# Performance work log

Measured on AMD Instinct MI355X. Metric: run time of the kernel, lower is better.

## Reference

```python
import jax, jax.numpy as jnp
import numpy as np
import math

LOG2PI = math.log(2.0 * math.pi)

def _silu(x):
    return x * jax.nn.sigmoid(x)

def _gru(x, W_ih, W_hh, b_ih, b_hh):
    # x: [B,T,X]; torch nn.GRU single layer, batch_first
    B = x.shape[0]
    H = W_hh.shape[1]
    gi_all = jnp.einsum('btx,gx->btg', x, W_ih) + b_ih  # [B,T,3H] input gates precomputed
    def step(h, gi):
        gh = h @ W_hh.T + b_hh
        i_r, i_z, i_n = jnp.split(gi, 3, axis=-1)
        h_r, h_z, h_n = jnp.split(gh, 3, axis=-1)
        r = jax.nn.sigmoid(i_r + h_r)
        z = jax.nn.sigmoid(i_z + h_z)
        n = jnp.tanh(i_n + r * h_n)
        h_new = (1.0 - z) * n + z * h
        return h_new, h_new
    h0 = jnp.zeros((B, H), x.dtype)
    h_last, h_seq = jax.lax.scan(step, h0, jnp.swapaxes(gi_all, 0, 1))
    return jnp.swapaxes(h_seq, 0, 1), h_last  # [B,T,H], [B,H]

def _A_Q(kappa, sigma, dt):
    A = jnp.exp(-kappa * dt)
    two_k_dt = 2.0 * kappa * dt
    small = (two_k_dt < 1e-6).astype(dt.dtype)
    Q_exact = sigma ** 2 * (1.0 - jnp.exp(-two_k_dt)) / jnp.maximum(2.0 * kappa, 1e-12)
    Q_taylor = sigma ** 2 * dt * (1.0 - kappa * dt + two_k_dt ** 2 / 6.0)
    Q = small * Q_taylor + (1.0 - small) * Q_exact
    return A, Q

def _ou_posterior(m0, s0, mu_k, A_k, Q_k, eps0, eps):
    B, Tm1, C = mu_k.shape
    c0 = m0 + s0 * eps0  # [B,C]
    s0c = jnp.maximum(s0, 1e-12)
    log_q0 = -0.5 * (((c0 - m0) / s0c) ** 2 + 2.0 * jnp.log(s0c) + LOG2PI).sum(-1)
    noise = eps * jnp.sqrt(jnp.maximum(Q_k, 1e-12))
    b = (1.0 - A_k) * mu_k + noise
    Phi_prefix = jnp.cumprod(A_k, axis=1)  # [B,T-1,C]
    Phi_full = jnp.concatenate([jnp.ones((B, 1, C), mu_k.dtype), Phi_prefix], axis=1)
    denom = jnp.maximum(Phi_full[:, 1:, :], 1e-20)
    s = b / denom
    S_full = jnp.concatenate([jnp.zeros((B, 1, C), mu_k.dtype), jnp.cumsum(s, axis=1)], axis=1)
    c = Phi_full * (c0[:, None, :] + S_full)  # [B,T,C]
    mean_trans = mu_k + A_k * (c[:, :-1, :] - mu_k)
    var_trans = jnp.maximum(Q_k, 1e-12)
    log_q_trans = -0.5 * ((c[:, 1:, :] - mean_trans) ** 2 / var_trans + jnp.log(var_trans) + LOG2PI)
    log_q = log_q0 + log_q_trans.sum(-1).sum(-1)
    return c, log_q

def reference(x, t, eps0, eps, W_ih, W_hh, b_ih, b_hh, Wi1, bi1, Wi2, bi2, Ws1, bs1, Ws2, bs2, Ws3, bs3):
    B, T, _ = x.shape
    h_seq, h_global = _gru(x, W_ih, W_hh, b_ih, b_hh)
    # soft time attention, temperature = 1.0
    delta = t[:, :, None, 0] - t[:, None, :, 0]  # [B,T,T]
    logits = -(T * delta) ** 2  # / tau^2 with tau=1
    w = jax.nn.softmax(logits, axis=-1)
    attn = jnp.einsum('bkj,bjh->bkh', w, h_seq)
    # init head
    h0_ctx = h_global + attn[:, 0, :]
    hi = _silu(h0_ctx @ Wi1.T + bi1)
    m0, logs0 = jnp.split(hi @ Wi2.T + bi2, 2, axis=-1)
    s0 = jax.nn.softplus(logs0) + 1e-6
    # step head on ctx[:, :-1]
    ctx = jnp.concatenate([h_global[:, None, :] + attn, t], axis=-1)[:, :-1, :]
    hs = _silu(ctx @ Ws1.T + bs1)
    hs = _silu(hs @ Ws2.T + bs2)
    params = hs @ Ws3.T + bs3
    mu_k, logk_k, logs_k = jnp.split(params, 3, axis=-1)
    kappa_k = jax.nn.softplus(logk_k) + 1e-6
    sigma_k = jax.nn.softplus(logs_k) + 1e-6
    dt = jnp.maximum(t[:, 1:, :] - t[:, :-1, :], 1e-6)
    A_k, Q_k = _A_Q(kappa_k, sigma_k, dt)
    c, log_q = _ou_posterior(m0, s0, mu_k, A_k, Q_k, eps0, eps)
    return c, log_q

def setup_inputs() -> dict:
    B, T, X, H, C = 8, 2048, 64, 256, 32
    key = jax.random.key(0)
    ks = jax.random.split(key, 16)
    def w(k, shape, scale=0.02):
        return (scale * jax.random.normal(k, shape)).astype(jnp.float32)
    x = jax.random.normal(ks[0], (B, T, X), dtype=jnp.float32)
    t = jnp.sort(jax.random.uniform(ks[1], (B, T, 1), dtype=jnp.float32), axis=1)
    eps0 = jax.random.normal(ks[2], (B, C), dtype=jnp.float32)
    eps = jax.random.normal(ks[3], (B, T - 1, C), dtype=jnp.float32)
    return {
        'x': x, 't': t, 'eps0': eps0, 'eps': eps,
        'W_ih': w(ks[4], (3 * H, X)), 'W_hh': w(ks[5], (3 * H, H)),
        'b_ih': jnp.zeros((3 * H,), jnp.float32), 'b_hh': jnp.zeros((3 * H,), jnp.float32),
        'Wi1': w(ks[6], (H, H)), 'bi1': jnp.zeros((H,), jnp.float32),
        'Wi2': w(ks[7], (2 * C, H)), 'bi2': jnp.zeros((2 * C,), jnp.float32),
        'Ws1': w(ks[8], (H, H + 1)), 'bs1': jnp.zeros((H,), jnp.float32),
        'Ws2': w(ks[9], (H, H)), 'bs2': jnp.zeros((H,), jnp.float32),
        'Ws3': w(ks[10], (3 * C, H)), 'bs3': jnp.zeros((3 * C,), jnp.float32),
    }
```

## Files before the change

kernel.cpp:

```cpp
#include <hip/hip_runtime.h>
#include <hip/hip_fp16.h>

#define LOG2PI_F 1.8378770664093453f

typedef _Float16 hf2_t __attribute__((ext_vector_type(2)));

#if defined(__has_builtin)
#  if __has_builtin(__builtin_amdgcn_fdot2)
#    define USE_FDOT2 1
#  endif
#endif
#ifndef USE_FDOT2
#  define USE_FDOT2 0
#endif

__device__ __forceinline__ float fdot2(unsigned int a, unsigned int b, float c) {
#if USE_FDOT2
  return __builtin_amdgcn_fdot2(__builtin_bit_cast(hf2_t, a),
                                __builtin_bit_cast(hf2_t, b), c, false);
#else
  __half2 ha = __builtin_bit_cast(__half2, a);
  __half2 hb = __builtin_bit_cast(__half2, b);
  float2 fa = __half22float2(ha);
  float2 fb = __half22float2(hb);
  return c + fa.x * fb.x + fa.y * fb.y;
#endif
}

__device__ __forceinline__ unsigned int packh2(float lo, float hi) {
  unsigned int l = (unsigned int)__half_as_ushort(__float2half(lo));
  unsigned int h = (unsigned int)__half_as_ushort(__float2half(hi));
  return (h << 16) | l;
}

__device__ __forceinline__ float sigmoid_f(float x) { return 1.f / (1.f + __expf(-x)); }
__device__ __forceinline__ float silu_f(float x) { return x * sigmoid_f(x); }
__device__ __forceinline__ float softplus_f(float x) {
  return fmaxf(x, 0.f) + log1pf(__expf(-fabsf(x)));
}
__device__ __forceinline__ float tanh_f(float x) {
  float ax = fabsf(x);
  float e = __expf(2.f * ax);
  return copysignf(1.f - 2.f / (e + 1.f), x);
}

__global__ void transpose_k(const float* __restrict__ in, float* __restrict__ out,
                            int R, int C) {
  int i = blockIdx.x * 256 + threadIdx.x;
  if (i < R * C) {
    int r = i / C, c = i % C;
    out[c * R + r] = in[i];
  }
}

__global__ void whh_pack(const float* __restrict__ W, unsigned int* __restrict__ WpkT) {
  int i = blockIdx.x * 256 + threadIdx.x;
  if (i < 98304) {
    int d = i / 768, g = i % 768;
    float lo = W[g * 256 + 2 * d];
    float hi = W[g * 256 + 2 * d + 1];
    WpkT[i] = packh2(lo, hi);
  }
}

__global__ void gi_gemm(const float* __restrict__ x, const float* __restrict__ WT,
                        const float* __restrict__ bih, float* __restrict__ gi) {
  int m0 = blockIdx.x * 8;
  int g = threadIdx.x;
  __shared__ float xs[8][64];
  for (int i = g; i < 512; i += 256) xs[i >> 6][i & 63] = x[m0 * 64 + i];
  __syncthreads();
  float b0 = bih[g], b1 = bih[g + 256], b2 = bih[g + 512];
  float a0[8], a1[8], a2[8];
#pragma unroll
  for (int r = 0; r < 8; r++) { a0[r] = b0; a1[r] = b1; a2[r] = b2; }
  for (int k = 0; k < 64; k++) {
    const float* w = WT + k * 768;
    float w0 = w[g], w1 = w[g + 256], w2 = w[g + 512];
#pragma unroll
    for (int r = 0; r < 8; r++) {
      float xv = xs[r][k];
      a0[r] = fmaf(w0, xv, a0[r]);
      a1[r] = fmaf(w1, xv, a1[r]);
      a2[r] = fmaf(w2, xv, a2[r]);
    }
  }
#pragma unroll
  for (int r = 0; r < 8; r++) {
    float* o = gi + (m0 + r) * 768;
    o[g] = a0[r];
    o[g + 256] = a1[r];
    o[g + 512] = a2[r];
  }
}

__global__ __launch_bounds__(768, 3) void gru_kernel(
    const unsigned int* __restrict__ WpkT,
    const float* __restrict__ gi,
    const float* __restrict__ bhh,
    float* __restrict__ h_seq)
{
  const int b = blockIdx.x;
  const int g = threadIdx.x;

  uint4 w[32];
#pragma unroll
  for (int i = 0; i < 32; i++) {
    int d = 4 * i;
    w[i] = make_uint4(WpkT[(d + 0) * 768 + g], WpkT[(d + 1) * 768 + g],
                      WpkT[(d + 2) * 768 + g], WpkT[(d + 3) * 768 + g]);
  }

  __shared__ __align__(16) unsigned int hpk[2][128];
  __shared__ float als[1024];
  if (g < 128) hpk[0][g] = 0u;

  const float bb = bhh[g];
  float h = 0.f;
  const float* gib = gi + b * 2048 * 768;
  float* hsb = h_seq + b * 2048 * 256;
  float gcur = gib[g];
  __syncthreads();

  for (int t = 0; t < 2048; t++) {
    float gnext = gib[min(t + 1, 2047) * 768 + g];

    const uint4* hp = (const uint4*)hpk[t & 1];
    float a = bb;
#pragma unroll
    for (int i = 0; i < 32; i++) {
      uint4 hv = hp[i];
      a = fdot2(w[i].x, hv.x, a);
      a = fdot2(w[i].y, hv.y, a);
      a = fdot2(w[i].z, hv.z, a);
      a = fdot2(w[i].w, hv.w, a);
    }
    if (g < 512) {
      als[g] = a + gcur;
    } else {
      als[g] = a;
      als[g + 256] = gcur;
    }
    __syncthreads();

    if (g < 256) {
      float rv = sigmoid_f(als[g]);
      float zv = sigmoid_f(als[256 + g]);
      float nv = tanh_f(als[768 + g] + rv * als[512 + g]);
      float hn = (1.f - zv) * nv + zv * h;
      h = hn;
      hsb[t * 256 + g] = hn;
      float other = __shfl_xor(hn, 1);
      if ((g & 1) == 0) hpk[(t + 1) & 1][g >> 1] = packh2(hn, other);
    }
    gcur = gnext;
    __syncthreads();
  }
}

#define AW 80
__global__ void attn_kernel(const float* __restrict__ h_seq, const float* __restrict__ t,
                            float* __restrict__ ctx) {
  const int blk = blockIdx.x;
  const int b = blk >> 7;
  const int k0 = (blk & 127) << 4;
  const int tid = threadIdx.x;

  __shared__ __align__(16) float ewT[176][16];
  __shared__ float ts[176];
  __shared__ float tks[16];
  __shared__ float rden[16];

  const float* tb = t + b * 2048;
  if (tid < 176) {
    int j = k0 - AW + tid;
    ts[tid] = tb[min(max(j, 0), 2047)];
  }
  if (tid < 16) tks[tid] = tb[k0 + tid];
  __syncthreads();

  for (int p = tid; p < 176 * 16; p += 256) {
    int kk = p & 15, jr = p >> 4;
    int j = k0 - AW + jr;
    float d = 2048.f * (tks[kk] - ts[jr]);
    float e = (j >= 0 && j < 2048) ? __expf(-d * d) : 0.f;
    ewT[jr][kk] = e;
  }
  __syncthreads();

  if (tid < 16) {
    float s = 0.f;
    for (int jr = 0; jr < 176; jr++) s += ewT[jr][tid];
    rden[tid] = 1.f / s;
  }
  __syncthreads();

  float acc[16];
#pragma unroll
  for (int kk = 0; kk < 16; kk++) acc[kk] = 0.f;

  const float* hb = h_seq + b * 2048 * 256;
  for (int jr = 0; jr < 176; jr++) {
    int j = min(max(k0 - AW + jr, 0), 2047);
    float hv = hb[j * 256 + tid];
    const float4* e4 = (const float4*)ewT[jr];
    float4 e0 = e4[0], e1 = e4[1], e2 = e4[2], e3 = e4[3];
    acc[0] = fmaf(e0.x, hv, acc[0]);   acc[1] = fmaf(e0.y, hv, acc[1]);
    acc[2] = fmaf(e0.z, hv, acc[2]);   acc[3] = fmaf(e0.w, hv, acc[3]);
    acc[4] = fmaf(e1.x, hv, acc[4]);   acc[5] = fmaf(e1.y, hv, acc[5]);
    acc[6] = fmaf(e1.z, hv, acc[6]);   acc[7] = fmaf(e1.w, hv, acc[7]);
    acc[8] = fmaf(e2.x, hv, acc[8]);   acc[9] = fmaf(e2.y, hv, acc[9]);
    acc[10] = fmaf(e2.z, hv, acc[10]); acc[11] = fmaf(e2.w, hv, acc[11]);
    acc[12] = fmaf(e3.x, hv, acc[12]); acc[13] = fmaf(e3.y, hv, acc[13]);
    acc[14] = fmaf(e3.z, hv, acc[14]); acc[15] = fmaf(e3.w, hv, acc[15]);
  }

  float hg = hb[2047 * 256 + tid];
  float* cb = ctx + (b * 2048 + k0) * 256 + tid;
#pragma unroll
  for (int kk = 0; kk < 16; kk++) cb[kk * 256] = hg + acc[kk] * rden[kk];
}

__global__ void init_head(const float* __restrict__ ctx, const float* __restrict__ WT1,
                          const float* __restrict__ bi1, const float* __restrict__ WT2,
                          const float* __restrict__ bi2, const float* __restrict__ eps0,
                          float* __restrict__ m0s0, float* __restrict__ lq0) {
  int b = blockIdx.x;
  int g = threadIdx.x;
  __shared__ float xs[256], his[256], ms[64], red[32];
  xs[g] = ctx[(b * 2048) * 256 + g];
  __syncthreads();
  float acc = bi1[g];
#pragma unroll 8
  for (int k = 0; k < 256; k++) acc = fmaf(WT1[k * 256 + g], xs[k], acc);
  his[g] = silu_f(acc);
  __syncthreads();
  if (g < 64) {
    float a2 = bi2[g];
#pragma unroll 8
    for (int k = 0; k < 256; k++) a2 = fmaf(WT2[k * 64 + g], his[k], a2);
    float v = (g < 32) ? a2 : (softplus_f(a2) + 1e-6f);
    m0s0[b * 64 + g] = v;
    ms[g] = v;
  }
  __syncthreads();
  if (g < 32) {
    float m = ms[g], s = ms[32 + g];
    float c0 = m + s * eps0[b * 32 + g];
    float sc = fmaxf(s, 1e-12f);
    float z = (c0 - m) / sc;
    red[g] = z * z + 2.f * __logf(sc) + LOG2PI_F;
  }
  __syncthreads();
  if (g == 0) {
    float s = 0.f;
    for (int i = 0; i < 32; i++) s += red[i];
    lq0[b] = -0.5f * s;
  }
}

__global__ void head_layer(const float* __restrict__ A, const float* __restrict__ WT,
                           const float* __restrict__ bias, const float* __restrict__ wext,
                           const float* __restrict__ tvec, float* __restrict__ C,
                           int N, int act) {
  int m0 = blockIdx.x * 8;
  int g = threadIdx.x;
  __shared__ __align__(16) float As[8][256];
#pragma unroll
  for (int r = 0; r < 8; r++) As[r][g] = A[(m0 + r) * 256 + g];
  __syncthreads();
  if (g < N) {
    float b0 = bias[g];
    float acc[8] = {b0, b0, b0, b0, b0, b0, b0, b0};
    for (int k4 = 0; k4 < 64; k4++) {
      const float* w = WT + (k4 * 4) * N + g;
      float w0v = w[0], w1v = w[N], w2v = w[2 * N], w3v = w[3 * N];
#pragma unroll
      for (int r = 0; r < 8; r++) {
        float4 xv = *(const float4*)(&As[r][k4 * 4]);
        acc[r] = fmaf(w0v, xv.x, acc[r]);
        acc[r] = fmaf(w1v, xv.y, acc[r]);
        acc[r] = fmaf(w2v, xv.z, acc[r]);
        acc[r] = fmaf(w3v, xv.w, acc[r]);
      }
    }
#pragma unroll
    for (int r = 0; r < 8; r++) {
      float a = acc[r];
      if (wext) a = fmaf(tvec[m0 + r], wext[g], a);
      if (act) a = silu_f(a);
      C[(m0 + r) * N + g] = a;
    }
  }
}

__global__ __launch_bounds__(1024) void ou_kernel(
    const float* __restrict__ params, const float* __restrict__ t,
    const float* __restrict__ eps, const float* __restrict__ eps0,
    const float* __restrict__ m0s0, const float* __restrict__ lq0,
    float* __restrict__ out) {
  const int b = blockIdx.x;
  const int c = threadIdx.x & 31;
  const int s = threadIdx.x >> 5;
  const int k0 = s * 64;
  const int k1 = min(k0 + 64, 2047);
  const float* tb = t + b * 2048;

  __shared__ float Ps[32][33], Ss[32][33], Cs[32][33], lqs[32][33];

  float P = 1.f, S = 0.f, lq = 0.f;
  for (int k = k0; k < k1; k++) {
    const float* pr = params + (b * 2048 + k) * 96;
    float mu = pr[c];
    float kap = softplus_f(pr[32 + c]) + 1e-6f;
    float sg = softplus_f(pr[64 + c]) + 1e-6f;
    float dt = fmaxf(tb[k + 1] - tb[k], 1e-6f);
    float A = __expf(-kap * dt);
    float tkd = 2.f * kap * dt;
    float Qe = sg * sg * (1.f - A * A) / fmaxf(2.f * kap, 1e-12f);
    float kd = kap * dt;
    float Qt = sg * sg * dt * (1.f - kd + tkd * tkd * (1.f / 6.f));
    float var = fmaxf((tkd < 1e-6f) ? Qt : Qe, 1e-12f);
    float e = eps[(b * 2047 + k) * 32 + c];
    float d = mu * (1.f - A) + e * sqrtf(var);
    S = fmaf(A, S, d);
    P *= A;
    lq += e * e + __logf(var) + LOG2PI_F;
  }
  Ps[c][s] = P;
  Ss[c][s] = S;
  lqs[c][s] = lq;
  __syncthreads();

  if (s == 0) {
    float m0v = m0s0[b * 64 + c];
    float s0v = m0s0[b * 64 + 32 + c];
    float cc = fmaf(s0v, eps0[b * 32 + c], m0v);
    out[(b * 2048) * 32 + c] = cc;
    float lqt = 0.f;
    for (int i = 0; i < 32; i++) {
      Cs[c][i] = cc;
      cc = fmaf(Ps[c][i], cc, Ss[c][i]);
      lqt += lqs[c][i];
    }
    for (int off = 16; off >= 1; off >>= 1) lqt += __shfl_down(lqt, off, 32);
    if (c == 0) out[8 * 2048 * 32 + b] = lq0[b] - 0.5f * lqt;
  }
  __syncthreads();

  float cc = Cs[c][s];
  for (int k = k0; k < k1; k++) {
    const float* pr = params + (b * 2048 + k) * 96;
    float mu = pr[c];
    float kap = softplus_f(pr[32 + c]) + 1e-6f;
    float sg = softplus_f(pr[64 + c]) + 1e-6f;
    float dt = fmaxf(tb[k + 1] - tb[k], 1e-6f);
    float A = __expf(-kap * dt);
    float tkd = 2.f * kap * dt;
    float Qe = sg * sg * (1.f - A * A) / fmaxf(2.f * kap, 1e-12f);
    float kd = kap * dt;
    float Qt = sg * sg * dt * (1.f - kd + tkd * tkd * (1.f / 6.f));
    float var = fmaxf((tkd < 1e-6f) ? Qt : Qe, 1e-12f);
    float e = eps[(b * 2047 + k) * 32 + c];
    float d = mu * (1.f - A) + e * sqrtf(var);
    cc = fmaf(A, cc, d);
    out[(b * 2048 + k + 1) * 32 + c] = cc;
  }
}

extern "C" void kernel_launch(void* const* d_in, const int* in_sizes, int n_in,
                              void* d_out, int out_size, void* d_ws, size_t ws_size,
                              hipStream_t stream) {
  (void)in_sizes; (void)n_in; (void)out_size; (void)ws_size;
  const float* x    = (const float*)d_in[0];
  const float* t    = (const float*)d_in[1];
  const float* eps0 = (const float*)d_in[2];
  const float* eps  = (const float*)d_in[3];
  const float* W_ih = (const float*)d_in[4];
  const float* W_hh = (const float*)d_in[5];
  const float* b_ih = (const float*)d_in[6];
  const float* b_hh = (const float*)d_in[7];
  const float* Wi1  = (const float*)d_in[8];
  const float* bi1  = (const float*)d_in[9];
  const float* Wi2  = (const float*)d_in[10];
  const float* bi2  = (const float*)d_in[11];
  const float* Ws1  = (const float*)d_in[12];
  const float* bs1  = (const float*)d_in[13];
  const float* Ws2  = (const float*)d_in[14];
  const float* bs2  = (const float*)d_in[15];
  const float* Ws3  = (const float*)d_in[16];
  const float* bs3  = (const float*)d_in[17];
  float* out = (float*)d_out;
  float* ws = (float*)d_ws;

  float*        WT_ih = ws + 0;
  unsigned int* WpkT  = (unsigned int*)(ws + 49152);
  float*        WT1   = ws + 147456;
  float*        WT2   = ws + 212992;
  float*        WTs1  = ws + 229376;
  float*        WTs2  = ws + 295168;
  float*        WTs3  = ws + 360704;
  float*        m0s0  = ws + 385280;
  float*        lq0   = ws + 385792;
  float*        gi    = ws + 385800;
  float*        h_seq = gi + 12582912;
  float*        ctx   = h_seq + 4194304;
  float*        hs1    = gi;
  float*        hs2    = gi + 4194304;
  float*        params = gi + 8388608;

  transpose_k<<<(768 * 64 + 255) / 256, 256, 0, stream>>>(W_ih, WT_ih, 768, 64);
  transpose_k<<<(256 * 256 + 255) / 256, 256, 0, stream>>>(Wi1, WT1, 256, 256);
  transpose_k<<<(64 * 256 + 255) / 256, 256, 0, stream>>>(Wi2, WT2, 64, 256);
  transpose_k<<<(256 * 257 + 255) / 256, 256, 0, stream>>>(Ws1, WTs1, 256, 257);
  transpose_k<<<(256 * 256 + 255) / 256, 256, 0, stream>>>(Ws2, WTs2, 256, 256);
  transpose_k<<<(96 * 256 + 255) / 256, 256, 0, stream>>>(Ws3, WTs3, 96, 256);
  whh_pack<<<384, 256, 0, stream>>>(W_hh, WpkT);

  gi_gemm<<<2048, 256, 0, stream>>>(x, WT_ih, b_ih, gi);
  gru_kernel<<<8, 768, 0, stream>>>(WpkT, gi, b_hh, h_seq);
  attn_kernel<<<1024, 256, 0, stream>>>(h_seq, t, ctx);
  init_head<<<8, 256, 0, stream>>>(ctx, WT1, bi1, WT2, bi2, eps0, m0s0, lq0);
  head_layer<<<2048, 256, 0, stream>>>(ctx, WTs1, bs1, WTs1 + 256 * 256, t, hs1, 256, 1);
  head_layer<<<2048, 256, 0, stream>>>(hs1, WTs2, bs2, nullptr, nullptr, hs2, 256, 1);
  head_layer<<<2048, 256, 0, stream>>>(hs2, WTs3, bs3, nullptr, nullptr, params, 96, 0);
  ou_kernel<<<8, 1024, 0, stream>>>(params, t, eps, eps0, m0s0, lq0, out);
}
```

Before: 3.156 ms.

## Fuse weight prep and head MLP layers, split GRU hidden n-gate across 512 threads

Merges the seven weight transpose/pack launches into one prep kernel. Fuses the three head MLP layers with the per-step OU coefficient computation, so intermediates stay in shared memory and the OU kernel only reads precomputed A, D and log terms instead of recomputing softplus/exp twice. Reworks the GRU recurrence to use 512 threads per block instead of 768, with each thread computing one full gate row plus half of an n-gate row, and the r gate kept in registers. The GRU change adds register pressure (48 uint4 per thread) and an extra shared-memory sum for the split dot product.

```diff
diff --git a/kernel.cpp b/kernel.cpp
--- a/kernel.cpp
+++ b/kernel.cpp
@@ -44,22 +44,39 @@
   return copysignf(1.f - 2.f / (e + 1.f), x);
 }
 
-__global__ void transpose_k(const float* __restrict__ in, float* __restrict__ out,
-                            int R, int C) {
-  int i = blockIdx.x * 256 + threadIdx.x;
+__device__ __forceinline__ void tr_piece(const float* in, float* out, int R, int C,
+                                         int i) {
   if (i < R * C) {
     int r = i / C, c = i % C;
     out[c * R + r] = in[i];
   }
 }
 
-__global__ void whh_pack(const float* __restrict__ W, unsigned int* __restrict__ WpkT) {
-  int i = blockIdx.x * 256 + threadIdx.x;
-  if (i < 98304) {
-    int d = i / 768, g = i % 768;
-    float lo = W[g * 256 + 2 * d];
-    float hi = W[g * 256 + 2 * d + 1];
-    WpkT[i] = packh2(lo, hi);
+__global__ void prep_kernel(const float* W_ih, const float* Wi1, const float* Wi2,
+                            const float* Ws1, const float* Ws2, const float* Ws3,
+                            const float* W_hh, float* WT_ih, float* WT1, float* WT2,
+                            float* WTs1, float* WTs2, float* WTs3,
+                            unsigned int* WpkT) {
+  int blk = blockIdx.x;
+  int tid = threadIdx.x;
+  if (blk < 192) {
+    tr_piece(W_ih, WT_ih, 768, 64, blk * 256 + tid);
+  } else if (blk < 448) {
+    tr_piece(Wi1, WT1, 256, 256, (blk - 192) * 256 + tid);
+  } else if (blk < 512) {
+    tr_piece(Wi2, WT2, 64, 256, (blk - 448) * 256 + tid);
+  } else if (blk < 769) {
+    tr_piece(Ws1, WTs1, 256, 257, (blk - 512) * 256 + tid);
+  } else if (blk < 1025) {
+    tr_piece(Ws2, WTs2, 256, 256, (blk - 769) * 256 + tid);
+  } else if (blk < 1121) {
+    tr_piece(Ws3, WTs3, 96, 256, (blk - 1025) * 256 + tid);
+  } else {
+    int i = (blk - 1121) * 256 + tid;
+    if (i < 98304) {
+      int d = i / 768, g = i % 768;
+      WpkT[i] = packh2(W_hh[g * 256 + 2 * d], W_hh[g * 256 + 2 * d + 1]);
+    }
   }
 }
 
@@ -94,66 +111,121 @@
   }
 }
 
-__global__ __launch_bounds__(768, 3) void gru_kernel(
+__global__ __launch_bounds__(512, 2) void gru_kernel(
     const unsigned int* __restrict__ WpkT,
     const float* __restrict__ gi,
     const float* __restrict__ bhh,
     float* __restrict__ h_seq)
 {
   const int b = blockIdx.x;
-  const int g = threadIdx.x;
-
-  uint4 w[32];
+  const int tid = threadIdx.x;
+  const int d = tid & 255;
+  const int half = tid >> 8;
+  const int nrow = 512 + d;
+
+  uint4 wf[32], wh[16];
 #pragma unroll
   for (int i = 0; i < 32; i++) {
-    int d = 4 * i;
-    w[i] = make_uint4(WpkT[(d + 0) * 768 + g], WpkT[(d + 1) * 768 + g],
-                      WpkT[(d + 2) * 768 + g], WpkT[(d + 3) * 768 + g]);
+    int dk = 4 * i;
+    wf[i] = make_uint4(WpkT[(dk + 0) * 768 + tid], WpkT[(dk + 1) * 768 + tid],
+                       WpkT[(dk + 2) * 768 + tid], WpkT[(dk + 3) * 768 + tid]);
+  }
+#pragma unroll
+  for (int i = 0; i < 16; i++) {
+    int dk = half * 64 + 4 * i;
+    wh[i] = make_uint4(WpkT[(dk + 0) * 768 + nrow], WpkT[(dk + 1) * 768 + nrow],
+                       WpkT[(dk + 2) * 768 + nrow], WpkT[(dk + 3) * 768 + nrow]);
+  }
+#pragma unroll
+  for (int i = 0; i < 32; i++) {
+    asm volatile("" : "+v"(wf[i].x), "+v"(wf[i].y), "+v"(wf[i].z), "+v"(wf[i].w));
+  }
+#pragma unroll
+  for (int i = 0; i < 16; i++) {
+    asm volatile("" : "+v"(wh[i].x), "+v"(wh[i].y), "+v"(wh[i].z), "+v"(wh[i].w));
   }
 
   __shared__ __align__(16) unsigned int hpk[2][128];
-  __shared__ float als[1024];
-  if (g < 128) hpk[0][g] = 0u;
-
-  const float bb = bhh[g];
+  __shared__ float als[768];
+  if (tid < 128) hpk[0][tid] = 0u;
+
+  const float bf = bhh[tid];
+  const float bh = (half == 0) ? bhh[nrow] : 0.f;
   float h = 0.f;
   const float* gib = gi + b * 2048 * 768;
   float* hsb = h_seq + b * 2048 * 256;
-  float gcur = gib[g];
+  float gcur = gib[tid];
+  float gncur = (tid < 256) ? gib[512 + tid] : 0.f;
   __syncthreads();
 
   for (int t = 0; t < 2048; t++) {
-    float gnext = gib[min(t + 1, 2047) * 768 + g];
+    int tn = min(t + 1, 2047);
+    float gnext = gib[tn * 768 + tid];
+    float gnnext = (tid < 256) ? gib[tn * 768 + 512 + tid] : 0.f;
 
     const uint4* hp = (const uint4*)hpk[t & 1];
-    float a = bb;
-#pragma unroll
-    for (int i = 0; i < 32; i++) {
-      uint4 hv = hp[i];
-      a = fdot2(w[i].x, hv.x, a);
-      a = fdot2(w[i].y, hv.y, a);
-      a = fdot2(w[i].z, hv.z, a);
-      a = fdot2(w[i].w, hv.w, a);
-    }
-    if (g < 512) {
-      als[g] = a + gcur;
+    float af = bf, ah = bh;
+    if (half == 0) {
+#pragma unroll
+      for (int i = 0; i < 16; i++) {
+        uint4 hv = hp[i];
+        af = fdot2(wf[i].x, hv.x, af);
+        af = fdot2(wf[i].y, hv.y, af);
+        af = fdot2(wf[i].z, hv.z, af);
+        af = fdot2(wf[i].w, hv.w, af);
+        ah = fdot2(wh[i].x, hv.x, ah);
+        ah = fdot2(wh[i].y, hv.y, ah);
+        ah = fdot2(wh[i].z, hv.z, ah);
+        ah = fdot2(wh[i].w, hv.w, ah);
+      }
+#pragma unroll
+      for (int i = 16; i < 32; i++) {
+        uint4 hv = hp[i];
+        af = fdot2(wf[i].x, hv.x, af);
+        af = fdot2(wf[i].y, hv.y, af);
+        af = fdot2(wf[i].z, hv.z, af);
+        af = fdot2(wf[i].w, hv.w, af);
+      }
     } else {
-      als[g] = a;
-      als[g + 256] = gcur;
-    }
+#pragma unroll
+      for (int i = 0; i < 16; i++) {
+        uint4 hv = hp[i];
+        af = fdot2(wf[i].x, hv.x, af);
+        af = fdot2(wf[i].y, hv.y, af);
+        af = fdot2(wf[i].z, hv.z, af);
+        af = fdot2(wf[i].w, hv.w, af);
+      }
+#pragma unroll
+      for (int i = 16; i < 32; i++) {
+        uint4 hv = hp[i];
+        af = fdot2(wf[i].x, hv.x, af);
+        af = fdot2(wf[i].y, hv.y, af);
+        af = fdot2(wf[i].z, hv.z, af);
+        af = fdot2(wf[i].w, hv.w, af);
+        ah = fdot2(wh[i - 16].x, hv.x, ah);
+        ah = fdot2(wh[i - 16].y, hv.y, ah);
+        ah = fdot2(wh[i - 16].z, hv.z, ah);
+        ah = fdot2(wh[i - 16].w, hv.w, ah);
+      }
+    }
+
+    if (tid >= 256) als[tid - 256] = af + gcur;
+    als[256 + tid] = ah;
     __syncthreads();
 
-    if (g < 256) {
-      float rv = sigmoid_f(als[g]);
-      float zv = sigmoid_f(als[256 + g]);
-      float nv = tanh_f(als[768 + g] + rv * als[512 + g]);
+    if (tid < 256) {
+      float rv = sigmoid_f(af + gcur);
+      float zv = sigmoid_f(als[d]);
+      float npart = als[256 + d] + als[512 + d];
+      float nv = tanh_f(gncur + rv * npart);
       float hn = (1.f - zv) * nv + zv * h;
       h = hn;
-      hsb[t * 256 + g] = hn;
+      hsb[t * 256 + d] = hn;
       float other = __shfl_xor(hn, 1);
-      if ((g & 1) == 0) hpk[(t + 1) & 1][g >> 1] = packh2(hn, other);
+      if ((d & 1) == 0) hpk[(t + 1) & 1][d >> 1] = packh2(hn, other);
     }
     gcur = gnext;
+    gncur = gnnext;
     __syncthreads();
   }
 }
@@ -259,22 +331,31 @@
   }
 }
 
-__global__ void head_layer(const float* __restrict__ A, const float* __restrict__ WT,
-                           const float* __restrict__ bias, const float* __restrict__ wext,
-                           const float* __restrict__ tvec, float* __restrict__ C,
-                           int N, int act) {
+__global__ __launch_bounds__(256) void head_fused(
+    const float* __restrict__ ctx, const float* __restrict__ WTs1,
+    const float* __restrict__ bs1, const float* __restrict__ WTs2,
+    const float* __restrict__ bs2, const float* __restrict__ WTs3,
+    const float* __restrict__ bs3, const float* __restrict__ t,
+    const float* __restrict__ eps, float* __restrict__ Aarr,
+    float* __restrict__ Darr, float* __restrict__ Larr) {
   int m0 = blockIdx.x * 8;
   int g = threadIdx.x;
   __shared__ __align__(16) float As[8][256];
-#pragma unroll
-  for (int r = 0; r < 8; r++) As[r][g] = A[(m0 + r) * 256 + g];
-  __syncthreads();
-  if (g < N) {
-    float b0 = bias[g];
+  __shared__ __align__(16) float Bs[8][256];
+  __shared__ float Ps[8][96];
+  __shared__ float trow[8];
+
+#pragma unroll
+  for (int r = 0; r < 8; r++) As[r][g] = ctx[(m0 + r) * 256 + g];
+  if (g < 8) trow[g] = t[m0 + g];
+  __syncthreads();
+
+  {
+    float b0 = bs1[g];
     float acc[8] = {b0, b0, b0, b0, b0, b0, b0, b0};
     for (int k4 = 0; k4 < 64; k4++) {
-      const float* w = WT + (k4 * 4) * N + g;
-      float w0v = w[0], w1v = w[N], w2v = w[2 * N], w3v = w[3 * N];
+      const float* w = WTs1 + (k4 * 4) * 256 + g;
+      float w0v = w[0], w1v = w[256], w2v = w[512], w3v = w[768];
 #pragma unroll
       for (int r = 0; r < 8; r++) {
         float4 xv = *(const float4*)(&As[r][k4 * 4]);
@@ -284,19 +365,79 @@
         acc[r] = fmaf(w3v, xv.w, acc[r]);
       }
     }
-#pragma unroll
-    for (int r = 0; r < 8; r++) {
-      float a = acc[r];
-      if (wext) a = fmaf(tvec[m0 + r], wext[g], a);
-      if (act) a = silu_f(a);
-      C[(m0 + r) * N + g] = a;
+    float we = WTs1[256 * 256 + g];
+#pragma unroll
+    for (int r = 0; r < 8; r++) Bs[r][g] = silu_f(fmaf(trow[r], we, acc[r]));
+  }
+  __syncthreads();
+
+  {
+    float b0 = bs2[g];
+    float acc[8] = {b0, b0, b0, b0, b0, b0, b0, b0};
+    for (int k4 = 0; k4 < 64; k4++) {
+      const float* w = WTs2 + (k4 * 4) * 256 + g;
+      float w0v = w[0], w1v = w[256], w2v = w[512], w3v = w[768];
+#pragma unroll
+      for (int r = 0; r < 8; r++) {
+        float4 xv = *(const float4*)(&Bs[r][k4 * 4]);
+        acc[r] = fmaf(w0v, xv.x, acc[r]);
+        acc[r] = fmaf(w1v, xv.y, acc[r]);
+        acc[r] = fmaf(w2v, xv.z, acc[r]);
+        acc[r] = fmaf(w3v, xv.w, acc[r]);
+      }
+    }
+#pragma unroll
+    for (int r = 0; r < 8; r++) As[r][g] = silu_f(acc[r]);
+  }
+  __syncthreads();
+
+  if (g < 96) {
+    float b0 = bs3[g];
+    float acc[8] = {b0, b0, b0, b0, b0, b0, b0, b0};
+    for (int k4 = 0; k4 < 64; k4++) {
+      const float* w = WTs3 + (k4 * 4) * 96 + g;
+      float w0v = w[0], w1v = w[96], w2v = w[192], w3v = w[288];
+#pragma unroll
+      for (int r = 0; r < 8; r++) {
+        float4 xv = *(const float4*)(&As[r][k4 * 4]);
+        acc[r] = fmaf(w0v, xv.x, acc[r]);
+        acc[r] = fmaf(w1v, xv.y, acc[r]);
+        acc[r] = fmaf(w2v, xv.z, acc[r]);
+        acc[r] = fmaf(w3v, xv.w, acc[r]);
+      }
+    }
+#pragma unroll
+    for (int r = 0; r < 8; r++) Ps[r][g] = acc[r];
+  }
+  __syncthreads();
+
+  {
+    int r = g >> 5, c = g & 31;
+    int k = m0 + r;
+    int b = k >> 11, kk = k & 2047;
+    if (kk < 2047) {
+      float mu = Ps[r][c];
+      float kap = softplus_f(Ps[r][32 + c]) + 1e-6f;
+      float sg = softplus_f(Ps[r][64 + c]) + 1e-6f;
+      float dt = fmaxf(t[k + 1] - t[k], 1e-6f);
+      float A = __expf(-kap * dt);
+      float tkd = 2.f * kap * dt;
+      float Qe = sg * sg * (1.f - A * A) / fmaxf(2.f * kap, 1e-12f);
+      float kd = kap * dt;
+      float Qt = sg * sg * dt * (1.f - kd + tkd * tkd * (1.f / 6.f));
+      float var = fmaxf((tkd < 1e-6f) ? Qt : Qe, 1e-12f);
+      float e = eps[(b * 2047 + kk) * 32 + c];
+      int idx = (b * 2047 + kk) * 32 + c;
+      Aarr[idx] = A;
+      Darr[idx] = fmaf(mu, 1.f - A, e * sqrtf(var));
+      Larr[idx] = e * e + __logf(var) + LOG2PI_F;
     }
   }
 }
 
 __global__ __launch_bounds__(1024) void ou_kernel(
-    const float* __restrict__ params, const float* __restrict__ t,
-    const float* __restrict__ eps, const float* __restrict__ eps0,
+    const float* __restrict__ Aarr, const float* __restrict__ Darr,
+    const float* __restrict__ Larr, const float* __restrict__ eps0,
     const float* __restrict__ m0s0, const float* __restrict__ lq0,
     float* __restrict__ out) {
   const int b = blockIdx.x;
@@ -304,28 +445,17 @@
   const int s = threadIdx.x >> 5;
   const int k0 = s * 64;
   const int k1 = min(k0 + 64, 2047);
-  const float* tb = t + b * 2048;
 
   __shared__ float Ps[32][33], Ss[32][33], Cs[32][33], lqs[32][33];
 
   float P = 1.f, S = 0.f, lq = 0.f;
   for (int k = k0; k < k1; k++) {
-    const float* pr = params + (b * 2048 + k) * 96;
-    float mu = pr[c];
-    float kap = softplus_f(pr[32 + c]) + 1e-6f;
-    float sg = softplus_f(pr[64 + c]) + 1e-6f;
-    float dt = fmaxf(tb[k + 1] - tb[k], 1e-6f);
-    float A = __expf(-kap * dt);
-    float tkd = 2.f * kap * dt;
-    float Qe = sg * sg * (1.f - A * A) / fmaxf(2.f * kap, 1e-12f);
-    float kd = kap * dt;
-    float Qt = sg * sg * dt * (1.f - kd + tkd * tkd * (1.f / 6.f));
-    float var = fmaxf((tkd < 1e-6f) ? Qt : Qe, 1e-12f);
-    float e = eps[(b * 2047 + k) * 32 + c];
-    float d = mu * (1.f - A) + e * sqrtf(var);
+    int idx = (b * 2047 + k) * 32 + c;
+    float A = Aarr[idx];
+    float d = Darr[idx];
     S = fmaf(A, S, d);
     P *= A;
-    lq += e * e + __logf(var) + LOG2PI_F;
+    lq += Larr[idx];
   }
   Ps[c][s] = P;
   Ss[c][s] = S;
@@ -350,20 +480,8 @@
 
   float cc = Cs[c][s];
   for (int k = k0; k < k1; k++) {
-    const float* pr = params + (b * 2048 + k) * 96;
-    float mu = pr[c];
-    float kap = softplus_f(pr[32 + c]) + 1e-6f;
-    float sg = softplus_f(pr[64 + c]) + 1e-6f;
-    float dt = fmaxf(tb[k + 1] - tb[k], 1e-6f);
-    float A = __expf(-kap * dt);
-    float tkd = 2.f * kap * dt;
-    float Qe = sg * sg * (1.f - A * A) / fmaxf(2.f * kap, 1e-12f);
-    float kd = kap * dt;
-    float Qt = sg * sg * dt * (1.f - kd + tkd * tkd * (1.f / 6.f));
-    float var = fmaxf((tkd < 1e-6f) ? Qt : Qe, 1e-12f);
-    float e = eps[(b * 2047 + k) * 32 + c];
-    float d = mu * (1.f - A) + e * sqrtf(var);
-    cc = fmaf(A, cc, d);
+    int idx = (b * 2047 + k) * 32 + c;
+    cc = fmaf(Aarr[idx], cc, Darr[idx]);
     out[(b * 2048 + k + 1) * 32 + c] = cc;
   }
 }
@@ -405,24 +523,17 @@
   float*        gi    = ws + 385800;
   float*        h_seq = gi + 12582912;
   float*        ctx   = h_seq + 4194304;
-  float*        hs1    = gi;
-  float*        hs2    = gi + 4194304;
-  float*        params = gi + 8388608;
-
-  transpose_k<<<(768 * 64 + 255) / 256, 256, 0, stream>>>(W_ih, WT_ih, 768, 64);
-  transpose_k<<<(256 * 256 + 255) / 256, 256, 0, stream>>>(Wi1, WT1, 256, 256);
-  transpose_k<<<(64 * 256 + 255) / 256, 256, 0, stream>>>(Wi2, WT2, 64, 256);
-  transpose_k<<<(256 * 257 + 255) / 256, 256, 0, stream>>>(Ws1, WTs1, 256, 257);
-  transpose_k<<<(256 * 256 + 255) / 256, 256, 0, stream>>>(Ws2, WTs2, 256, 256);
-  transpose_k<<<(96 * 256 + 255) / 256, 256, 0, stream>>>(Ws3, WTs3, 96, 256);
-  whh_pack<<<384, 256, 0, stream>>>(W_hh, WpkT);
-
+  float*        Aarr = gi;
+  float*        Darr = gi + 524032;
+  float*        Larr = gi + 1048064;
+
+  prep_kernel<<<1505, 256, 0, stream>>>(W_ih, Wi1, Wi2, Ws1, Ws2, Ws3, W_hh,
+                                        WT_ih, WT1, WT2, WTs1, WTs2, WTs3, WpkT);
   gi_gemm<<<2048, 256, 0, stream>>>(x, WT_ih, b_ih, gi);
-  gru_kernel<<<8, 768, 0, stream>>>(WpkT, gi, b_hh, h_seq);
+  gru_kernel<<<8, 512, 0, stream>>>(WpkT, gi, b_hh, h_seq);
   attn_kernel<<<1024, 256, 0, stream>>>(h_seq, t, ctx);
   init_head<<<8, 256, 0, stream>>>(ctx, WT1, bi1, WT2, bi2, eps0, m0s0, lq0);
-  head_layer<<<2048, 256, 0, stream>>>(ctx, WTs1, bs1, WTs1 + 256 * 256, t, hs1, 256, 1);
-  head_layer<<<2048, 256, 0, stream>>>(hs1, WTs2, bs2, nullptr, nullptr, hs2, 256, 1);
-  head_layer<<<2048, 256, 0, stream>>>(hs2, WTs3, bs3, nullptr, nullptr, params, 96, 0);
-  ou_kernel<<<8, 1024, 0, stream>>>(params, t, eps, eps0, m0s0, lq0, out);
-}
+  head_fused<<<2048, 256, 0, stream>>>(ctx, WTs1, bs1, WTs2, bs2, WTs3, bs3, t, eps,
+                                       Aarr, Darr, Larr);
+  ou_kernel<<<8, 1024, 0, stream>>>(Aarr, Darr, Larr, eps0, m0s0, lq0, out);
+}
```

Measured after the change: 6.927 ms. 120% more time.
